# Kernel optimization log

Measured on AMD Instinct MI355X. Metric: run time of the kernel, lower is better.

## Reference

```python
import jax, jax.numpy as jnp
import numpy as np

B, N, HID, NHEADS, VOCAB = 8, 2048, 768, 4, 15
ALPHA = 0.2  # LeakyReLU negative slope
NEG = -9e15  # matches -9000000000000000.0 mask constant


def setup_inputs() -> dict:
    key = jax.random.key(0)
    ks = jax.random.split(key, 7)
    node_feats = jax.random.randint(ks[0], (B, N), 0, VOCAB, dtype=jnp.int32)
    adjs = jax.random.randint(ks[1], (B, N, N), 0, 2, dtype=jnp.int32)
    embed_table = jax.random.normal(ks[2], (VOCAB, HID), dtype=jnp.float32)
    W_heads = jax.random.normal(ks[3], (NHEADS, HID, HID), dtype=jnp.float32) * 0.05
    a_heads = jax.random.normal(ks[4], (NHEADS, 2 * HID, 1), dtype=jnp.float32) * 0.05
    W_out = jax.random.normal(ks[5], (NHEADS * HID, HID), dtype=jnp.float32) * 0.05
    a_out = jax.random.normal(ks[6], (2 * HID, 1), dtype=jnp.float32) * 0.05
    return {"node_feats": node_feats, "adjs": adjs, "embed_table": embed_table,
            "W_heads": W_heads, "a_heads": a_heads, "W_out": W_out, "a_out": a_out}


def gat_layer(h, adj, W, a, concat):
    # h: (B,N,Fin), adj: (B,N,N), W: (Fin,Fout), a: (2*Fout,1)
    Fout = W.shape[1]
    Wh = jnp.matmul(h, W)                      # (B,N,Fout)
    Wh1 = jnp.matmul(Wh, a[:Fout])             # (B,N,1)
    Wh2 = jnp.matmul(Wh, a[Fout:])             # (B,N,1)
    e = Wh1 + jnp.swapaxes(Wh2, 1, 2)          # (B,N,N)
    e = jax.nn.leaky_relu(e, negative_slope=ALPHA)
    e = jnp.where(adj > 0, e, NEG)
    att = jax.nn.softmax(e, axis=-1)           # (B,N,N)
    h_prime = jnp.matmul(att, Wh)              # (B,N,Fout)
    return jax.nn.elu(h_prime) if concat else h_prime


def reference(node_feats, adjs, embed_table, W_heads, a_heads, W_out, a_out):
    x = embed_table[node_feats]                # (B,N,HID)  (shape_enc treated as identity)
    # multi-head GAT, heads vmapped then concatenated along feature dim
    heads = jax.vmap(lambda W, a: gat_layer(x, adjs, W, a, concat=True))(W_heads, a_heads)
    x = jnp.concatenate(jnp.moveaxis(heads, 0, -2).reshape(B, N, 1, NHEADS * HID).squeeze(2)[None], axis=0)[0] if False else jnp.transpose(heads, (1, 2, 0, 3)).reshape(B, N, NHEADS * HID)
    x = jax.nn.elu(gat_layer(x, adjs, W_out, a_out, concat=False))  # (B,N,HID)
    # pooling_forward with all-ones mask -> masked mean over node dim
    sum_emb = jnp.sum(x, axis=1)               # (B,HID)
    denom = jnp.maximum(jnp.full_like(sum_emb, float(N)), 1e-9)
    return sum_emb / denom                     # (B,HID)
```

## Files before the change

### kernel.cpp

```cpp
#include <hip/hip_runtime.h>
#include <math.h>

#define BB 8
#define NN 2048
#define HID 768
#define NHEADS 4
#define VOCAB 15
#define ALPHA 0.2f
#define NEGV -9e15f
#define MTOT (BB * NN)

using short4v = __attribute__((ext_vector_type(4))) short;
using short8v = __attribute__((ext_vector_type(8))) short;
using f32x4 = __attribute__((ext_vector_type(4))) float;

__device__ __forceinline__ short f2bf(float f) {
  union { float f; unsigned u; } x;
  x.f = f;
  unsigned r = x.u + 0x7fffu + ((x.u >> 16) & 1u);
  return (short)(r >> 16);
}

__device__ __forceinline__ void cp16(const void* g, void* l) {
  __builtin_amdgcn_global_load_lds(
      (const __attribute__((address_space(1))) unsigned int*)g,
      (__attribute__((address_space(3))) unsigned int*)l, 16, 0, 0);
}

#define PACK_B 131072
#define ZERO_B 308
#define NFM_B 64
#define TRAN_B 2304
__global__ __launch_bounds__(256) void setup_kernel(
    const int* __restrict__ adj, unsigned long long* __restrict__ packed,
    float* __restrict__ zbase, const int* __restrict__ nf,
    unsigned long long* __restrict__ nfm, const float* __restrict__ W_out,
    short* __restrict__ Wt_o) {
  const int bid = blockIdx.x;
  const int tid = threadIdx.x;
  if (bid < PACK_B) {
    long idx = (long)bid * 256 + tid;
    unsigned long long m = __ballot(adj[idx] > 0);
    if ((tid & 63) == 0) packed[idx >> 6] = m;
  } else if (bid < PACK_B + ZERO_B) {
    zbase[(bid - PACK_B) * 256 + tid] = 0.f;
  } else if (bid < PACK_B + ZERO_B + NFM_B) {
    int r = bid - PACK_B - ZERO_B;
    int b = r >> 3, c = r & 7;
    int w = tid >> 6;
    int j = c * 256 + tid;
    int nfv = nf[b * NN + j];
#pragma unroll
    for (int v = 0; v < VOCAB; ++v) {
      unsigned long long m = __ballot(nfv == v);
      if ((tid & 63) == 0) nfm[((long)b * VOCAB + v) * 32 + c * 4 + w] = m;
    }
  } else {
    __shared__ float t[32][33];
    int r2 = bid - PACK_B - ZERO_B - NFM_B;
    const int K = NHEADS * HID, N = HID;
    int k0 = (r2 % 96) * 32, n0 = (r2 / 96) * 32;
    int tx = tid & 31, ty = tid >> 5;
#pragma unroll
    for (int i = 0; i < 32; i += 8)
      t[ty + i][tx] = W_out[(long)(k0 + ty + i) * N + n0 + tx];
    __syncthreads();
#pragma unroll
    for (int i = 0; i < 32; i += 8)
      Wt_o[(long)(n0 + ty + i) * K + k0 + tx] = f2bf(t[tx][ty + i]);
  }
}

__global__ __launch_bounds__(256) void tw_kernel(
    const float* __restrict__ table, const float* __restrict__ W_heads,
    float* __restrict__ TW) {
  __shared__ float tbl[VOCAB][48];
  const int c = blockIdx.x * 256 + threadIdx.x;
  const int h = (blockIdx.x * 256) / HID;
  const int n = c - h * HID;
  const int k0 = blockIdx.y * 48;
  for (int idx = threadIdx.x; idx < VOCAB * 48; idx += 256)
    tbl[idx / 48][idx % 48] = table[(idx / 48) * HID + k0 + idx % 48];
  __syncthreads();
  float acc[VOCAB];
#pragma unroll
  for (int v = 0; v < VOCAB; ++v) acc[v] = 0.f;
  const float* wp = W_heads + (long)h * HID * HID + (long)k0 * HID + n;
#pragma unroll 8
  for (int kk = 0; kk < 48; ++kk) {
    float w = wp[(long)kk * HID];
#pragma unroll
    for (int v = 0; v < VOCAB; ++v) acc[v] = fmaf(tbl[v][kk], w, acc[v]);
  }
#pragma unroll
  for (int v = 0; v < VOCAB; ++v) atomicAdd(&TW[v * (NHEADS * HID) + c], acc[v]);
}

__global__ __launch_bounds__(256) void tw12_kernel(
    const float* __restrict__ TW, const float* __restrict__ a_heads,
    float* __restrict__ TW1, float* __restrict__ TW2) {
  int h = blockIdx.x / VOCAB, v = blockIdx.x % VOCAB;
  const float* twr = TW + v * (NHEADS * HID) + h * HID;
  const float* a1 = a_heads + h * 2 * HID;
  float s1 = 0.f, s2 = 0.f;
  for (int n = threadIdx.x; n < HID; n += 256) {
    float t = twr[n];
    s1 = fmaf(t, a1[n], s1);
    s2 = fmaf(t, a1[HID + n], s2);
  }
  __shared__ float r1[256], r2[256];
  r1[threadIdx.x] = s1;
  r2[threadIdx.x] = s2;
  __syncthreads();
  for (int s = 128; s > 0; s >>= 1) {
    if (threadIdx.x < s) {
      r1[threadIdx.x] += r1[threadIdx.x + s];
      r2[threadIdx.x] += r2[threadIdx.x + s];
    }
    __syncthreads();
  }
  if (threadIdx.x == 0) {
    TW1[h * VOCAB + v] = r1[0];
    TW2[h * VOCAB + v] = r2[0];
  }
}

__global__ __launch_bounds__(256) void p16_kernel(
    const int* __restrict__ nf, const unsigned* __restrict__ padj32,
    const unsigned* __restrict__ nfm32, const float* __restrict__ TW1,
    const float* __restrict__ TW2, float* __restrict__ P16) {
  const int t = threadIdx.x;
  const int wv = t >> 6;
  const int lane = t & 63;
  const int rowm = blockIdx.x * 4 + wv;
  const int b = rowm >> 11;
  __shared__ float cnts[4][16];

  unsigned a = padj32[(long)rowm * 64 + lane];
  const unsigned* nb = nfm32 + (long)b * VOCAB * 64 + lane;
  int cnt[VOCAB];
#pragma unroll
  for (int v = 0; v < VOCAB; ++v) cnt[v] = __popc(a & nb[v * 64]);
#pragma unroll
  for (int off = 1; off < 64; off <<= 1)
#pragma unroll
    for (int v = 0; v < VOCAB; ++v) cnt[v] += __shfl_xor(cnt[v], off);
  int cntsum = 0;
#pragma unroll
  for (int v = 0; v < VOCAB; ++v) cntsum += cnt[v];
  const bool use_full = (cntsum == 0);
  if (use_full) {
#pragma unroll
    for (int v = 0; v < VOCAB; ++v) cnt[v] = __popc(nb[v * 64]);
#pragma unroll
    for (int off = 1; off < 64; off <<= 1)
#pragma unroll
      for (int v = 0; v < VOCAB; ++v) cnt[v] += __shfl_xor(cnt[v], off);
  }
  if (lane < 16) cnts[wv][lane] = (lane < VOCAB) ? (float)cnt[lane] : 0.f;
  __syncthreads();

  const int h = lane >> 4;
  const int v = lane & 15;
  const int nfi = nf[b * NN + (rowm & 2047)];
  float cvf = cnts[wv][v];
  bool valid = (v < VOCAB) && (cvf > 0.f);
  float logit = 0.f;
  if (!use_full) {
    float s = TW1[h * VOCAB + nfi] + ((v < VOCAB) ? TW2[h * VOCAB + v] : 0.f);
    logit = s > 0.f ? s : ALPHA * s;
  }
  float mv = valid ? logit : -INFINITY;
#pragma unroll
  for (int off = 1; off < 16; off <<= 1) mv = fmaxf(mv, __shfl_xor(mv, off));
  float pv = valid ? cvf * __expf(logit - mv) : 0.f;
  float sum = pv;
#pragma unroll
  for (int off = 1; off < 16; off <<= 1) sum += __shfl_xor(sum, off);
  if (v < VOCAB) P16[((long)h * 16384 + rowm) * 16 + v] = pv / sum;
}

__global__ __launch_bounds__(256) void hcat_expand(
    const float* __restrict__ TW, const float* __restrict__ P16,
    short* __restrict__ hcat) {
  __shared__ float twl[VOCAB * 128];
  __shared__ float pl[128 * 16];
  const int c0 = blockIdx.x * 128;
  const int r0 = blockIdx.y * 128;
  const int h = c0 / HID;
  const int t = threadIdx.x;
  for (int idx = t; idx < VOCAB * 128; idx += 256)
    twl[idx] = TW[(idx / 128) * (NHEADS * HID) + c0 + (idx & 127)];
  for (int idx = t; idx < 128 * 16; idx += 256)
    pl[idx] = P16[((long)h * 16384 + r0 + (idx >> 4)) * 16 + (idx & 15)];
  __syncthreads();
  const int clb = (t & 31) * 4;
  const int rlb = (t >> 5) * 16;
#pragma unroll 4
  for (int rr = 0; rr < 16; ++rr) {
    int rl = rlb + rr;
    short4v o;
#pragma unroll
    for (int cc = 0; cc < 4; ++cc) {
      float s = 0.f;
#pragma unroll
      for (int vv = 0; vv < VOCAB; ++vv)
        s = fmaf(pl[rl * 16 + vv], twl[vv * 128 + clb + cc], s);
      s = s > 0.f ? s : (__expf(s) - 1.f);
      o[cc] = f2bf(s);
    }
    *(short4v*)(hcat + (long)(r0 + rl) * (NHEADS * HID) + c0 + clb) = o;
  }
}

template <int MODE>
__global__ __launch_bounds__(256, 4) void mfma_gemm(
    const short* __restrict__ A, const short* __restrict__ B,
    int K, int lda, int ldb, long sA, long sB,
    float* __restrict__ Cf, short* __restrict__ Ct,
    const float* __restrict__ a_vec, float* __restrict__ Wh1g,
    float* __restrict__ Wh2g) {
  __shared__ short smem[8704];
  short* As = smem;
  short* Bs = smem + 4096;

  const int gx = gridDim.x, gy = gridDim.y;
  int lin = blockIdx.x + gx * (blockIdx.y + gy * blockIdx.z);
  const int per = (gx * gy * gridDim.z) >> 3;
  int work = (lin & 7) * per + (lin >> 3);
  const int bx = work % gx;
  int tmp = work / gx;
  const int by = tmp % gy;
  const int z = tmp / gy;

  A += (long)z * sA;
  B += (long)z * sB;

  const int tid = threadIdx.x;
  const int m0 = by * 128;
  const int n0 = bx * 128;

  const int lane = tid & 63;
  const int wid = tid >> 6;
  const int wm = (wid & 1) * 64;
  const int wn = (wid >> 1) * 64;
  const int l15 = lane & 15;
  const int quad = lane >> 4;
  const int cp = quad ^ ((l15 >> 1) & 3);

  f32x4 acc[4][4];
#pragma unroll
  for (int i = 0; i < 4; ++i)
#pragma unroll
    for (int j = 0; j < 4; ++j) acc[i][j] = (f32x4){0.f, 0.f, 0.f, 0.f};

  for (int k0 = 0; k0 < K; k0 += 32) {
#pragma unroll
    for (int it = 0; it < 2; ++it) {
      int lin2 = it * 256 + tid;
      int r = lin2 >> 2;
      int p = lin2 & 3;
      int kc = p ^ ((r >> 1) & 3);
      cp16(A + (long)(m0 + r) * lda + k0 + kc * 8, &As[lin2 * 8]);
    }
#pragma unroll
    for (int it = 0; it < 2; ++it) {
      int lin2 = it * 256 + tid;
      int r = lin2 >> 2;
      int p = lin2 & 3;
      int kc = p ^ ((r >> 1) & 3);
      cp16(B + (long)(n0 + r) * ldb + k0 + kc * 8, &Bs[lin2 * 8]);
    }
    __syncthreads();

    short8v af[4], bfr[4];
#pragma unroll
    for (int i = 0; i < 4; ++i)
      af[i] = *(const short8v*)(As + (wm + i * 16 + l15) * 32 + cp * 8);
#pragma unroll
    for (int j = 0; j < 4; ++j)
      bfr[j] = *(const short8v*)(Bs + (wn + j * 16 + l15) * 32 + cp * 8);
#pragma unroll
    for (int i = 0; i < 4; ++i)
#pragma unroll
      for (int j = 0; j < 4; ++j)
        acc[i][j] = __builtin_amdgcn_mfma_f32_16x16x32_bf16(af[i], bfr[j],
                                                            acc[i][j], 0, 0, 0);
    __syncthreads();
  }

  if constexpr (MODE == 3) {
#pragma unroll
    for (int j = 0; j < 4; ++j) {
      int col = n0 + wn + j * 16 + l15;
      float s = 0.f;
#pragma unroll
      for (int i = 0; i < 4; ++i)
#pragma unroll
        for (int reg = 0; reg < 4; ++reg) {
          float v = acc[i][j][reg];
          s += v > 0.f ? v : (__expf(v) - 1.f);
        }
      s += __shfl_xor(s, 16);
      s += __shfl_xor(s, 32);
      if (quad == 0) atomicAdd(Cf + (long)z * HID + col, s * (1.0f / NN));
    }
  } else {
    float a1v[4], a2v[4];
#pragma unroll
    for (int j = 0; j < 4; ++j) {
      int colh = n0 + wn + j * 16 + l15;
      a1v[j] = a_vec[colh];
      a2v[j] = a_vec[HID + colh];
    }
#pragma unroll
    for (int i = 0; i < 4; ++i) {
      int rb = m0 + wm + i * 16 + quad * 4;
#pragma unroll
      for (int reg = 0; reg < 4; ++reg) {
        float s1 = 0.f, s2 = 0.f;
#pragma unroll
        for (int j = 0; j < 4; ++j) {
          s1 = fmaf(acc[i][j][reg], a1v[j], s1);
          s2 = fmaf(acc[i][j][reg], a2v[j], s2);
        }
#pragma unroll
        for (int off = 1; off < 16; off <<= 1) {
          s1 += __shfl_xor(s1, off);
          s2 += __shfl_xor(s2, off);
        }
        if (l15 == 0) {
          atomicAdd(Wh1g + rb + reg, s1);
          atomicAdd(Wh2g + rb + reg, s2);
        }
      }
    }
    const int bb = m0 >> 11;
    const int ml0 = m0 & 2047;
#pragma unroll
    for (int p = 0; p < 2; ++p) {
      if (wn == p * 64) {
#pragma unroll
        for (int j = 0; j < 4; ++j) {
          int col_l = j * 16 + l15;
#pragma unroll
          for (int i = 0; i < 4; ++i) {
            int row_l = wm + i * 16 + quad * 4;
            short4v pk;
#pragma unroll
            for (int reg = 0; reg < 4; ++reg) pk[reg] = f2bf(acc[i][j][reg]);
            *(short4v*)(smem + col_l * 136 + row_l) = pk;
          }
        }
      }
      __syncthreads();
#pragma unroll
      for (int it = 0; it < 4; ++it) {
        int idx = it * 256 + tid;
        int col_l = idx >> 4;
        int ch = idx & 15;
        short8v ld = *(const short8v*)(smem + col_l * 136 + ch * 8);
        int colh = n0 + p * 64 + col_l;
        *(short8v*)(Ct + ((long)bb * HID + colh) * NN + ml0 + ch * 8) = ld;
      }
      __syncthreads();
    }
  }
}

__global__ __launch_bounds__(256) void attn_softmax_kernel(
    const float* __restrict__ Wh1, const float* __restrict__ Wh2,
    const unsigned long long* __restrict__ packed, short* __restrict__ att,
    float* __restrict__ zA, int zn) {
  int row = blockIdx.x;
  if (row < zn) zA[row * 256 + threadIdx.x] = 0.f;
  int b = row >> 11;
  const unsigned char* bits = (const unsigned char*)(packed + (long)row * 32);
  const float* wh2b = Wh2 + b * NN;
  const int t = threadIdx.x;
  const int lane = t & 63;
  const int wv = t >> 6;

  unsigned m8 = bits[t];
  float wh1 = Wh1[row];
  float4 wa = ((const float4*)(wh2b + t * 8))[0];
  float4 wb = ((const float4*)(wh2b + t * 8))[1];
  float v[8] = {wa.x, wa.y, wa.z, wa.w, wb.x, wb.y, wb.z, wb.w};

  float lmax = -INFINITY;
#pragma unroll
  for (int k = 0; k < 8; ++k) {
    float s = wh1 + v[k];
    s = s > 0.f ? s : ALPHA * s;
    s = ((m8 >> k) & 1u) ? s : NEGV;
    v[k] = s;
    lmax = fmaxf(lmax, s);
  }

  __shared__ float redm[4], reds[4];
#pragma unroll
  for (int off = 32; off > 0; off >>= 1) lmax = fmaxf(lmax, __shfl_xor(lmax, off));
  if (lane == 0) redm[wv] = lmax;
  __syncthreads();
  float m = fmaxf(fmaxf(redm[0], redm[1]), fmaxf(redm[2], redm[3]));

  float lsum = 0.f;
#pragma unroll
  for (int k = 0; k < 8; ++k) {
    float p = __expf(v[k] - m);
    v[k] = p;
    lsum += p;
  }
#pragma unroll
  for (int off = 32; off > 0; off >>= 1) lsum += __shfl_xor(lsum, off);
  if (lane == 0) reds[wv] = lsum;
  __syncthreads();
  float inv = 1.f / (reds[0] + reds[1] + reds[2] + reds[3]);

  short8v o;
#pragma unroll
  for (int k = 0; k < 8; ++k) o[k] = f2bf(v[k] * inv);
  *(short8v*)(att + (long)row * NN + t * 8) = o;
}

extern "C" void kernel_launch(void* const* d_in, const int* in_sizes, int n_in,
                              void* d_out, int out_size, void* d_ws,
                              size_t ws_size, hipStream_t stream) {
  const int* node_feats = (const int*)d_in[0];
  const int* adjs = (const int*)d_in[1];
  const float* embed_table = (const float*)d_in[2];
  const float* W_heads = (const float*)d_in[3];
  const float* a_heads = (const float*)d_in[4];
  const float* W_out = (const float*)d_in[5];
  const float* a_out = (const float*)d_in[6];
  float* out = (float*)d_out;

  char* p = (char*)d_ws;
  short* Wt_o = (short*)p;  p += (size_t)HID * (NHEADS * HID) * 2;
  short* Wh_t = (short*)p;  p += (size_t)BB * HID * NN * 2;
  short* att2 = (short*)p;  p += (size_t)BB * NN * NN * 2;
  short* hcat = (short*)p;  p += (size_t)MTOT * NHEADS * HID * 2;
  unsigned long long* padj = (unsigned long long*)p;
  p += (size_t)BB * NN * NN / 8;
  float* P16 = (float*)p;   p += (size_t)NHEADS * 16384 * 16 * 4;
  float* Wh1 = (float*)p;   p += (size_t)16384 * 4;
  float* Wh2 = (float*)p;   p += (size_t)16384 * 4;
  float* TW = (float*)p;    p += (size_t)VOCAB * NHEADS * HID * 4;
  float* TW1 = (float*)p;   p += (size_t)NHEADS * VOCAB * 4;
  float* TW2 = (float*)p;   p += (size_t)NHEADS * VOCAB * 4;
  unsigned long long* nfm = (unsigned long long*)p;
  p += (size_t)BB * VOCAB * 32 * 8;
  if ((size_t)(p - (char*)d_ws) > ws_size) return;

  setup_kernel<<<PACK_B + ZERO_B + NFM_B + TRAN_B, 256, 0, stream>>>(
      adjs, padj, Wh1, node_feats, nfm, W_out, Wt_o);

  tw_kernel<<<dim3(12, 16), 256, 0, stream>>>(embed_table, W_heads, TW);
  tw12_kernel<<<NHEADS * VOCAB, 256, 0, stream>>>(TW, a_heads, TW1, TW2);
  p16_kernel<<<16384 / 4, 256, 0, stream>>>(
      node_feats, (const unsigned*)padj, (const unsigned*)nfm, TW1, TW2, P16);
  hcat_expand<<<dim3(24, 128), 256, 0, stream>>>(TW, P16, hcat);

  mfma_gemm<0><<<dim3(HID / 128, MTOT / 128, 1), 256, 0, stream>>>(
      hcat, Wt_o, NHEADS * HID, NHEADS * HID, NHEADS * HID, 0, 0,
      nullptr, Wh_t, a_out, Wh1, Wh2);
  attn_softmax_kernel<<<MTOT, 256, 0, stream>>>(Wh1, Wh2, padj, att2, out, 24);
  mfma_gemm<3><<<dim3(HID / 128, NN / 128, BB), 256, 0, stream>>>(
      att2, Wh_t, NN, NN, NN, (long)NN * NN, (long)HID * NN,
      out, nullptr, nullptr, nullptr, nullptr);
}
```

Measured before the change: 462.8 us.

## Fuse TW computation into setup kernel, coarsen adj packing, widen hcat stores

Moves the embedding-times-W_heads partial products into the setup kernel as extra blocks. Each block now writes its own partial slice instead of doing atomicAdd, and a small reduce kernel sums the 16 slices. This removes a separate launch and the atomic contention, and also removes the reliance on pre-zeroed TW. The adjacency bit-packing now has each block handle four ballot rounds, cutting the block count by four. hcat_expand writes 8 bf16 values per store instead of 4. The cost is extra workspace for partial sums and one extra small kernel launch.

```diff
diff --git a/kernel.cpp b/kernel.cpp
--- a/kernel.cpp
+++ b/kernel.cpp
@@ -27,21 +27,27 @@
       (__attribute__((address_space(3))) unsigned int*)l, 16, 0, 0);
 }
 
-#define PACK_B 131072
+#define PACK_B 32768
 #define ZERO_B 308
 #define NFM_B 64
 #define TRAN_B 2304
+#define TW_B 192
 __global__ __launch_bounds__(256) void setup_kernel(
     const int* __restrict__ adj, unsigned long long* __restrict__ packed,
     float* __restrict__ zbase, const int* __restrict__ nf,
     unsigned long long* __restrict__ nfm, const float* __restrict__ W_out,
-    short* __restrict__ Wt_o) {
+    short* __restrict__ Wt_o, const float* __restrict__ table,
+    const float* __restrict__ W_heads, float* __restrict__ TW) {
   const int bid = blockIdx.x;
   const int tid = threadIdx.x;
   if (bid < PACK_B) {
-    long idx = (long)bid * 256 + tid;
-    unsigned long long m = __ballot(adj[idx] > 0);
-    if ((tid & 63) == 0) packed[idx >> 6] = m;
+    long base = (long)bid * 1024;
+#pragma unroll
+    for (int r = 0; r < 4; ++r) {
+      long idx = base + r * 256 + tid;
+      unsigned long long m = __ballot(adj[idx] > 0);
+      if ((tid & 63) == 0) packed[idx >> 6] = m;
+    }
   } else if (bid < PACK_B + ZERO_B) {
     zbase[(bid - PACK_B) * 256 + tid] = 0.f;
   } else if (bid < PACK_B + ZERO_B + NFM_B) {
@@ -55,7 +61,7 @@
       unsigned long long m = __ballot(nfv == v);
       if ((tid & 63) == 0) nfm[((long)b * VOCAB + v) * 32 + c * 4 + w] = m;
     }
-  } else {
+  } else if (bid < PACK_B + ZERO_B + NFM_B + TRAN_B) {
     __shared__ float t[32][33];
     int r2 = bid - PACK_B - ZERO_B - NFM_B;
     const int K = NHEADS * HID, N = HID;
@@ -68,32 +74,44 @@
 #pragma unroll
     for (int i = 0; i < 32; i += 8)
       Wt_o[(long)(n0 + ty + i) * K + k0 + tx] = f2bf(t[tx][ty + i]);
-  }
-}
-
-__global__ __launch_bounds__(256) void tw_kernel(
-    const float* __restrict__ table, const float* __restrict__ W_heads,
-    float* __restrict__ TW) {
-  __shared__ float tbl[VOCAB][48];
+  } else {
+    __shared__ float tbl[VOCAB][48];
+    int r3 = bid - PACK_B - ZERO_B - NFM_B - TRAN_B;
+    const int cx = r3 % 12, ky = r3 / 12;
+    const int c = cx * 256 + tid;
+    const int h = (cx * 256) / HID;
+    const int n = c - h * HID;
+    const int k0 = ky * 48;
+    for (int idx = tid; idx < VOCAB * 48; idx += 256)
+      tbl[idx / 48][idx % 48] = table[(idx / 48) * HID + k0 + idx % 48];
+    __syncthreads();
+    float acc[VOCAB];
+#pragma unroll
+    for (int v = 0; v < VOCAB; ++v) acc[v] = 0.f;
+    const float* wp = W_heads + (long)h * HID * HID + (long)k0 * HID + n;
+#pragma unroll 8
+    for (int kk = 0; kk < 48; ++kk) {
+      float w = wp[(long)kk * HID];
+#pragma unroll
+      for (int v = 0; v < VOCAB; ++v) acc[v] = fmaf(tbl[v][kk], w, acc[v]);
+    }
+#pragma unroll
+    for (int v = 0; v < VOCAB; ++v)
+      TW[((long)ky * VOCAB + v) * (NHEADS * HID) + c] = acc[v];
+  }
+}
+
+__global__ __launch_bounds__(256) void tw_reduce_kernel(
+    const float* __restrict__ TWp, float* __restrict__ TW) {
   const int c = blockIdx.x * 256 + threadIdx.x;
-  const int h = (blockIdx.x * 256) / HID;
-  const int n = c - h * HID;
-  const int k0 = blockIdx.y * 48;
-  for (int idx = threadIdx.x; idx < VOCAB * 48; idx += 256)
-    tbl[idx / 48][idx % 48] = table[(idx / 48) * HID + k0 + idx % 48];
-  __syncthreads();
-  float acc[VOCAB];
-#pragma unroll
-  for (int v = 0; v < VOCAB; ++v) acc[v] = 0.f;
-  const float* wp = W_heads + (long)h * HID * HID + (long)k0 * HID + n;
-#pragma unroll 8
-  for (int kk = 0; kk < 48; ++kk) {
-    float w = wp[(long)kk * HID];
-#pragma unroll
-    for (int v = 0; v < VOCAB; ++v) acc[v] = fmaf(tbl[v][kk], w, acc[v]);
-  }
-#pragma unroll
-  for (int v = 0; v < VOCAB; ++v) atomicAdd(&TW[v * (NHEADS * HID) + c], acc[v]);
+#pragma unroll
+  for (int v = 0; v < VOCAB; ++v) {
+    float s = 0.f;
+#pragma unroll
+    for (int ky = 0; ky < 16; ++ky)
+      s += TWp[((long)ky * VOCAB + v) * (NHEADS * HID) + c];
+    TW[v * (NHEADS * HID) + c] = s;
+  }
 }
 
 __global__ __launch_bounds__(256) void tw12_kernel(
@@ -194,14 +212,14 @@
   for (int idx = t; idx < 128 * 16; idx += 256)
     pl[idx] = P16[((long)h * 16384 + r0 + (idx >> 4)) * 16 + (idx & 15)];
   __syncthreads();
-  const int clb = (t & 31) * 4;
-  const int rlb = (t >> 5) * 16;
-#pragma unroll 4
-  for (int rr = 0; rr < 16; ++rr) {
+  const int clb = (t & 15) * 8;
+  const int rlb = (t >> 4) * 8;
+#pragma unroll
+  for (int rr = 0; rr < 8; ++rr) {
     int rl = rlb + rr;
-    short4v o;
-#pragma unroll
-    for (int cc = 0; cc < 4; ++cc) {
+    short8v o;
+#pragma unroll
+    for (int cc = 0; cc < 8; ++cc) {
       float s = 0.f;
 #pragma unroll
       for (int vv = 0; vv < VOCAB; ++vv)
@@ -209,7 +227,7 @@
       s = s > 0.f ? s : (__expf(s) - 1.f);
       o[cc] = f2bf(s);
     }
-    *(short4v*)(hcat + (long)(r0 + rl) * (NHEADS * HID) + c0 + clb) = o;
+    *(short8v*)(hcat + (long)(r0 + rl) * (NHEADS * HID) + c0 + clb) = o;
   }
 }
 
@@ -445,6 +463,8 @@
   float* P16 = (float*)p;   p += (size_t)NHEADS * 16384 * 16 * 4;
   float* Wh1 = (float*)p;   p += (size_t)16384 * 4;
   float* Wh2 = (float*)p;   p += (size_t)16384 * 4;
+  p += (size_t)(ZERO_B * 256 - 2 * 16384) * 4;
+  float* TWp = (float*)p;   p += (size_t)16 * VOCAB * NHEADS * HID * 4;
   float* TW = (float*)p;    p += (size_t)VOCAB * NHEADS * HID * 4;
   float* TW1 = (float*)p;   p += (size_t)NHEADS * VOCAB * 4;
   float* TW2 = (float*)p;   p += (size_t)NHEADS * VOCAB * 4;
@@ -452,10 +472,11 @@
   p += (size_t)BB * VOCAB * 32 * 8;
   if ((size_t)(p - (char*)d_ws) > ws_size) return;
 
-  setup_kernel<<<PACK_B + ZERO_B + NFM_B + TRAN_B, 256, 0, stream>>>(
-      adjs, padj, Wh1, node_feats, nfm, W_out, Wt_o);
-
-  tw_kernel<<<dim3(12, 16), 256, 0, stream>>>(embed_table, W_heads, TW);
+  setup_kernel<<<PACK_B + ZERO_B + NFM_B + TRAN_B + TW_B, 256, 0, stream>>>(
+      adjs, padj, Wh1, node_feats, nfm, W_out, Wt_o, embed_table, W_heads,
+      TWp);
+
+  tw_reduce_kernel<<<12, 256, 0, stream>>>(TWp, TW);
   tw12_kernel<<<NHEADS * VOCAB, 256, 0, stream>>>(TW, a_heads, TW1, TW2);
   p16_kernel<<<16384 / 4, 256, 0, stream>>>(
       node_feats, (const unsigned*)padj, (const unsigned*)nfm, TW1, TW2, P16);
```

New measurement: 694.9 us. +50.2%, slower.
